# Performance work log

Measured on AMD Instinct MI355X. Metric: run time of the kernel, lower is better.

## Reference

```python
import jax, jax.numpy as jnp
import numpy as np

B, S, D, H = 2, 2048, 2048, 16
HD = D // H
QMAX = 127.0  # 8-bit activation quant


def ste_round(x):
    # forward: round; backward: identity
    return x + jax.lax.stop_gradient(jnp.round(x) - x)


def bitlinear(x, w):
    """BitNet b1.58 linear: per-tensor ternary weights + per-token int8 activations.

    x: [..., in], w: [out, in] -> [..., out]
    """
    w_scale = jnp.maximum(jnp.mean(jnp.abs(w)), 1e-6)
    w_q = jnp.clip(ste_round(w / w_scale), -1.0, 1.0)          # ternary {-1,0,1}
    a_max = jnp.clip(jnp.max(jnp.abs(x), axis=-1, keepdims=True), 1e-8, None)
    x_q = jnp.clip(ste_round(x * (QMAX / a_max)), -QMAX, QMAX)  # int8 range
    y = jnp.einsum('bsi,oi->bso', x_q, w_q)
    return y * (w_scale * a_max / QMAX)


def setup_inputs() -> dict:
    key = jax.random.key(0)
    ks = jax.random.split(key, 5)
    std = 1.0 / np.sqrt(D)  # muP-style init from BitLinear
    return {
        'x': jax.random.normal(ks[0], (B, S, D), dtype=jnp.float32),
        'wq': jax.random.normal(ks[1], (D, D), dtype=jnp.float32) * std,
        'wk': jax.random.normal(ks[2], (D, D), dtype=jnp.float32) * std,
        'wv': jax.random.normal(ks[3], (D, D), dtype=jnp.float32) * std,
        'wo': jax.random.normal(ks[4], (D, D), dtype=jnp.float32) * std,
    }


def reference(x, wq, wk, wv, wo):
    q = bitlinear(x, wq).reshape(B, S, H, HD)
    k = bitlinear(x, wk).reshape(B, S, H, HD)
    v = bitlinear(x, wv).reshape(B, S, H, HD)
    scores = jnp.einsum('bqhd,bkhd->bhqk', q, k) / np.sqrt(HD)
    # causal mask
    causal = jnp.tril(jnp.ones((S, S), dtype=bool))
    scores = jnp.where(causal[None, None], scores, jnp.finfo(scores.dtype).min)
    attn = jax.nn.softmax(scores, axis=-1)
    ctx = jnp.einsum('bhqk,bkhd->bqhd', attn, v).reshape(B, S, D)
    return bitlinear(ctx, wo)
```

## Files before the change

kernel.cpp:

```cpp
#include <hip/hip_runtime.h>
#include <hip/hip_bf16.h>
#include <cstdint>
#include <cstddef>


#define BB 2
#define SS 2048
#define DD 2048
#define HH 16
#define HDD 128
#define MM (BB*SS)

typedef __attribute__((ext_vector_type(8))) short bf16x8;
typedef __attribute__((ext_vector_type(4))) float f32x4;
typedef __attribute__((ext_vector_type(16))) float f32x16;
typedef __attribute__((ext_vector_type(4))) int   i32x4;
typedef unsigned short u16;
typedef unsigned int   u32;
typedef unsigned char  u8;
typedef signed char    s8;

#define MFMA(a,b,c)   __builtin_amdgcn_mfma_f32_16x16x32_bf16(a,b,c,0,0,0)
#define MFMA32(a,b,c) __builtin_amdgcn_mfma_f32_32x32x16_bf16(a,b,c,0,0,0)
#define MFMAI8(a,b,c) __builtin_amdgcn_mfma_i32_16x16x64_i8(a,b,c,0,0,0)

static __device__ __forceinline__ u16 f2bf(float f) {
  u32 x = __float_as_uint(f);
  u32 r = x + 0x7fffu + ((x >> 16) & 1u);
  return (u16)(r >> 16);
}

static __device__ __forceinline__ void gl_lds16(const void* g, void* l) {
  __builtin_amdgcn_global_load_lds((const __attribute__((address_space(1))) void*)g,
                                   (__attribute__((address_space(3))) void*)l, 16, 0, 0);
}

__global__ void k_wabs_partial(const float* __restrict__ w0, const float* __restrict__ w1,
                               const float* __restrict__ w2, const float* __restrict__ w3,
                               double* __restrict__ part) {
  int m = blockIdx.x >> 8, blk = blockIdx.x & 255;
  const float* w = (m == 0) ? w0 : (m == 1) ? w1 : (m == 2) ? w2 : w3;
  const float* p = w + (size_t)blk * 16384;
  double s = 0.0;
  for (int i = threadIdx.x * 4; i < 16384; i += 1024) {
    float4 v = *(const float4*)(p + i);
    s += (double)fabsf(v.x) + (double)fabsf(v.y) + (double)fabsf(v.z) + (double)fabsf(v.w);
  }
  __shared__ double red[256];
  red[threadIdx.x] = s;
  __syncthreads();
  for (int off = 128; off > 0; off >>= 1) {
    if ((int)threadIdx.x < off) red[threadIdx.x] += red[threadIdx.x + off];
    __syncthreads();
  }
  if (threadIdx.x == 0) part[m * 256 + blk] = red[0];
}

__global__ void k_wscale_final(const double* __restrict__ part, float* __restrict__ scales) {
  int m = threadIdx.x;
  if (m < 4) {
    double s = 0.0;
    for (int i = 0; i < 256; i++) s += part[m * 256 + i];
    float v = (float)(s * (1.0 / 4194304.0));
    scales[m] = fmaxf(v, 1e-6f);
  }
}

__global__ void k_wquant(const float* __restrict__ w0, const float* __restrict__ w1,
                         const float* __restrict__ w2, const float* __restrict__ w3,
                         s8* __restrict__ wq, const float* __restrict__ scales) {
  int m = blockIdx.y;
  const float* w = (m == 0) ? w0 : (m == 1) ? w1 : (m == 2) ? w2 : w3;
  float ws = scales[m];
  size_t i = ((size_t)blockIdx.x * 256 + threadIdx.x) * 4;
  float4 v = *(const float4*)(w + i);
  s8 o[4];
  o[0] = (s8)(int)fminf(1.f, fmaxf(-1.f, rintf(v.x / ws)));
  o[1] = (s8)(int)fminf(1.f, fmaxf(-1.f, rintf(v.y / ws)));
  o[2] = (s8)(int)fminf(1.f, fmaxf(-1.f, rintf(v.z / ws)));
  o[3] = (s8)(int)fminf(1.f, fmaxf(-1.f, rintf(v.w / ws)));
  *(int*)(wq + (size_t)m * DD * DD + i) = *(const int*)o;
}

__global__ __launch_bounds__(256) void k_rowquant(const float* __restrict__ x, s8* __restrict__ xq,
                                                  float* __restrict__ amax) {
  int row = blockIdx.x, t = threadIdx.x;
  const float* p = x + (size_t)row * DD + t * 8;
  float4 v0 = *(const float4*)(p);
  float4 v1 = *(const float4*)(p + 4);
  float m = fmaxf(fmaxf(fmaxf(fabsf(v0.x), fabsf(v0.y)), fmaxf(fabsf(v0.z), fabsf(v0.w))),
                  fmaxf(fmaxf(fabsf(v1.x), fabsf(v1.y)), fmaxf(fabsf(v1.z), fabsf(v1.w))));
  m = fmaxf(m, __shfl_xor(m, 1));  m = fmaxf(m, __shfl_xor(m, 2));
  m = fmaxf(m, __shfl_xor(m, 4));  m = fmaxf(m, __shfl_xor(m, 8));
  m = fmaxf(m, __shfl_xor(m, 16)); m = fmaxf(m, __shfl_xor(m, 32));
  __shared__ float red[4];
  if ((t & 63) == 0) red[t >> 6] = m;
  __syncthreads();
  m = fmaxf(fmaxf(red[0], red[1]), fmaxf(red[2], red[3]));
  m = fmaxf(m, 1e-8f);
  if (t == 0) amax[row] = m;
  float s = 127.0f / m;
  s8 o[8];
  o[0] = (s8)(int)fminf(127.f, fmaxf(-127.f, rintf(v0.x * s)));
  o[1] = (s8)(int)fminf(127.f, fmaxf(-127.f, rintf(v0.y * s)));
  o[2] = (s8)(int)fminf(127.f, fmaxf(-127.f, rintf(v0.z * s)));
  o[3] = (s8)(int)fminf(127.f, fmaxf(-127.f, rintf(v0.w * s)));
  o[4] = (s8)(int)fminf(127.f, fmaxf(-127.f, rintf(v1.x * s)));
  o[5] = (s8)(int)fminf(127.f, fmaxf(-127.f, rintf(v1.y * s)));
  o[6] = (s8)(int)fminf(127.f, fmaxf(-127.f, rintf(v1.z * s)));
  o[7] = (s8)(int)fminf(127.f, fmaxf(-127.f, rintf(v1.w * s)));
  *(uint2*)(xq + (size_t)row * DD + t * 8) = *(const uint2*)o;
}

template<bool OB, int NBNL>
__global__ __launch_bounds__(512) void k_gemm(const s8* __restrict__ A, const s8* __restrict__ Bw,
                                              const float* __restrict__ amax,
                                              const float* __restrict__ scales, int sbase,
                                              void* __restrict__ outv) {
  __shared__ alignas(16) u8 Asm[2][128 * 128];
  __shared__ alignas(16) u8 Bsm[2][256 * 128];
  int id = blockIdx.x;
  int xcd = id & 7, kk = id >> 3;
  int bm = kk & 31, bn = xcd * NBNL + (kk >> 5);
  int t = threadIdx.x, w = t >> 6, l = t & 63;
  int wr = w >> 2, wc = w & 3;
  int l15 = l & 15, lh = l >> 4;
  int r0 = t >> 3;
  int c0 = ((t & 7) ^ (r0 & 7)) * 16;
  const s8* Ab = A  + (size_t)(bm * 128) * DD;
  const s8* Bb = Bw + (size_t)(bn * 256) * DD;

#define STG_A(tt) do { u8* d_ = &Asm[(tt) & 1][0];                                    \
    gl_lds16(Ab + (size_t)r0 * DD + (tt) * 128 + c0,        d_ + t * 16);             \
    gl_lds16(Ab + (size_t)(r0 + 64) * DD + (tt) * 128 + c0, d_ + (512 + t) * 16); } while (0)
#define STG_B(tt, h_) do { u8* d_ = &Bsm[(tt) & 1][(h_) * 16384];                     \
    gl_lds16(Bb + (size_t)((h_) * 128 + r0) * DD + (tt) * 128 + c0,        d_ + t * 16);\
    gl_lds16(Bb + (size_t)((h_) * 128 + r0 + 64) * DD + (tt) * 128 + c0,   d_ + (512 + t) * 16); } while (0)

  i32x4 acc[4][4] = {};
  STG_A(0); STG_B(0, 0); STG_B(0, 1); STG_B(1, 0);
  asm volatile("s_waitcnt vmcnt(2)" ::: "memory");
  asm volatile("s_barrier" ::: "memory");
  for (int kb = 0; kb < 16; kb++) {
    int b = kb & 1;
    const u8* Ac = &Asm[b][0];
    const u8* Bc = &Bsm[b][0];
    i32x4 af[4][2], bf[2][2];
    #pragma unroll
    for (int i = 0; i < 4; i++)
      #pragma unroll
      for (int ks = 0; ks < 2; ks++)
        af[i][ks] = *(const i32x4*)(Ac + (wr * 64 + i * 16 + l15) * 128 + (((ks * 4 + lh) ^ (l15 & 7)) * 16));
    #pragma unroll
    for (int j = 0; j < 2; j++)
      #pragma unroll
      for (int ks = 0; ks < 2; ks++)
        bf[j][ks] = *(const i32x4*)(Bc + ((wc + 4 * j) * 16 + l15) * 128 + (((ks * 4 + lh) ^ (l15 & 7)) * 16));
    if (kb + 1 < 16) { STG_A(kb + 1); STG_B(kb + 1, 1); }
    asm volatile("s_barrier" ::: "memory");
    asm volatile("s_waitcnt lgkmcnt(0)" ::: "memory");
    __builtin_amdgcn_sched_barrier(0);
    __builtin_amdgcn_s_setprio(1);
    #pragma unroll
    for (int ks = 0; ks < 2; ks++)
      #pragma unroll
      for (int i = 0; i < 4; i++)
        #pragma unroll
        for (int j = 0; j < 2; j++)
          acc[i][j] = MFMAI8(af[i][ks], bf[j][ks], acc[i][j]);
    __builtin_amdgcn_s_setprio(0);
    asm volatile("s_barrier" ::: "memory");
    i32x4 bg[2][2];
    #pragma unroll
    for (int j = 0; j < 2; j++)
      #pragma unroll
      for (int ks = 0; ks < 2; ks++)
        bg[j][ks] = *(const i32x4*)(Bc + ((wc + 4 * (2 + j)) * 16 + l15) * 128 + (((ks * 4 + lh) ^ (l15 & 7)) * 16));
    if (kb + 2 < 16) STG_B(kb + 2, 0);
    asm volatile("s_barrier" ::: "memory");
    asm volatile("s_waitcnt lgkmcnt(0)" ::: "memory");
    __builtin_amdgcn_sched_barrier(0);
    __builtin_amdgcn_s_setprio(1);
    #pragma unroll
    for (int ks = 0; ks < 2; ks++)
      #pragma unroll
      for (int i = 0; i < 4; i++)
        #pragma unroll
        for (int j = 0; j < 2; j++)
          acc[i][2 + j] = MFMAI8(af[i][ks], bg[j][ks], acc[i][2 + j]);
    __builtin_amdgcn_s_setprio(0);
    if (kb < 14) {
      asm volatile("s_waitcnt vmcnt(2)" ::: "memory");
      asm volatile("s_barrier" ::: "memory");
    } else if (kb == 14) {
      asm volatile("s_waitcnt vmcnt(0)" ::: "memory");
      asm volatile("s_barrier" ::: "memory");
    }
  }
#undef STG_A
#undef STG_B
  int mz = OB ? (bn >> 3) : 0;
  int lcol0 = OB ? ((bn & 7) * 256) : (bn * 256);
  float wsc = scales[sbase + mz];
  u16*   outb = (u16*)outv + (size_t)mz * MM * DD;
  float* outf = (float*)outv;
  #pragma unroll
  for (int i = 0; i < 4; i++) {
    int row0 = bm * 128 + wr * 64 + i * 16 + lh * 4;
    #pragma unroll
    for (int r = 0; r < 4; r++) {
      float sc = (wsc * amax[row0 + r]) / 127.0f;
      #pragma unroll
      for (int j = 0; j < 4; j++) {
        int col = lcol0 + (wc + 4 * j) * 16 + l15;
        float y = (float)acc[i][j][r] * sc;
        if (OB) outb[(size_t)(row0 + r) * DD + col] = f2bf(y);
        else    outf[(size_t)(row0 + r) * DD + col] = y;
      }
    }
  }
}

__global__ __launch_bounds__(256) void k_vtrans(const u16* __restrict__ v, u16* __restrict__ vt) {
  __shared__ u16 tile[64][72];
  int sb = blockIdx.x;
  int db = blockIdx.y;
  int bh = blockIdx.z;
  int b = bh >> 4, h = bh & 15;
  int t = threadIdx.x;
  int ls = t >> 2, ld0 = (t & 3) * 16;
  const u16* src = v + (size_t)(b * SS + sb * 64 + ls) * DD + h * HDD + db * 64 + ld0;
  *(int4*)(&tile[ls][ld0])     = *(const int4*)(src);
  *(int4*)(&tile[ls][ld0 + 8]) = *(const int4*)(src + 8);
  __syncthreads();
  int d = t >> 2, s0 = (t & 3) * 16;
  u16 tmp[16];
  #pragma unroll
  for (int k = 0; k < 16; k++) tmp[k] = tile[s0 + k][d];
  u16* dst = vt + (size_t)((bh * HDD) + db * 64 + d) * SS + sb * 64 + s0;
  *(int4*)(dst)     = *(const int4*)(tmp);
  *(int4*)(dst + 8) = *(const int4*)(tmp + 8);
}

__global__ __launch_bounds__(128) void k_attn(const u16* __restrict__ Q, const u16* __restrict__ K,
                                              const u16* __restrict__ VT, float* __restrict__ O) {
  __shared__ u16 Ks[64 * 128];
  __shared__ u16 Vs[128 * 64];
  __shared__ u16 Ps[2 * 32 * 64];
  int id = blockIdx.x;
  int xcd = id & 7, rr = id >> 3;
  int bh = xcd * 4 + (rr & 3), pr = rr >> 2;
  int b = bh >> 4, h = bh & 15;
  int t = threadIdx.x, w = t >> 6, l = t & 63;
  int l31 = l & 31, hi = l >> 5;
  int l15 = l & 15, lh = l >> 4;
  size_t base = (size_t)(b * SS) * DD + h * HDD;
  const u16* vtb = VT + (size_t)bh * HDD * SS;
  u16* Ptw = Ps + w * 2048;
  const float sc = 0.08838834764831845f;
  int ksr[8], kso[8], vsr[8], vso[8];
  #pragma unroll
  for (int i = 0; i < 8; i++) {
    int s = i * 128 + t;
    ksr[i] = s >> 4; kso[i] = ((s & 15) ^ (ksr[i] & 15)) * 8;
    vsr[i] = s >> 3; vso[i] = ((s & 7) ^ (vsr[i] & 7)) * 8;
  }
  for (int half = 0; half < 2; half++) {
    int qt = half ? (31 - pr) : pr;
    int qrow = qt * 64 + w * 32 + l31;
    bf16x8 qf[8];
    #pragma unroll
    for (int kt = 0; kt < 8; kt++)
      qf[kt] = *(const bf16x8*)(Q + base + (size_t)qrow * DD + kt * 16 + hi * 8);
    f32x4 cacc[2][8] = {};
    float mrun = -INFINITY, lrun = 0.f;
    for (int kb = 0; kb <= qt; kb++) {
      #pragma unroll
      for (int i = 0; i < 8; i++)
        gl_lds16(K + base + (size_t)(kb * 64 + ksr[i]) * DD + kso[i], Ks + (i * 128 + t) * 8);
      #pragma unroll
      for (int i = 0; i < 8; i++)
        gl_lds16(vtb + (size_t)vsr[i] * SS + kb * 64 + vso[i], Vs + (i * 128 + t) * 8);
      __syncthreads();
      f32x16 c0 = {}, c1 = {};
      #pragma unroll
      for (int kt = 0; kt < 8; kt++) {
        int sl = (((kt * 2 + hi) ^ (l31 & 15)) * 8);
        bf16x8 kf0 = *(const bf16x8*)(Ks + l31 * 128 + sl);
        bf16x8 kf1 = *(const bf16x8*)(Ks + (32 + l31) * 128 + sl);
        c0 = MFMA32(kf0, qf[kt], c0);
        c1 = MFMA32(kf1, qf[kt], c1);
      }
      if (kb == qt) {
        #pragma unroll
        for (int rg = 0; rg < 16; rg++) {
          int kv0 = kb * 64 + (rg & 3) + 8 * (rg >> 2) + 4 * hi;
          if (kv0 > qrow)      c0[rg] = -1e30f;
          if (kv0 + 32 > qrow) c1[rg] = -1e30f;
        }
      }
      float ta[16];
      #pragma unroll
      for (int rg = 0; rg < 16; rg++) ta[rg] = fmaxf(c0[rg], c1[rg]);
      #pragma unroll
      for (int off = 8; off > 0; off >>= 1)
        #pragma unroll
        for (int rg = 0; rg < 8; rg++)
          if (rg < off) ta[rg] = fmaxf(ta[rg], ta[rg + off]);
      float pmax = fmaxf(ta[0], __shfl_xor(ta[0], 32));
      if (__any(pmax - mrun > 90.50967f)) {
        float mnew = fmaxf(mrun, pmax);
        float alpha = __expf((mrun - mnew) * sc);
        lrun *= alpha;
        #pragma unroll
        for (int m16 = 0; m16 < 2; m16++)
          #pragma unroll
          for (int r = 0; r < 4; r++) {
            float ar = __shfl(alpha, m16 * 16 + lh * 4 + r);
            #pragma unroll
            for (int n2 = 0; n2 < 8; n2++) cacc[m16][n2][r] *= ar;
          }
        mrun = mnew;
      }
      float msc = mrun * sc;
      float ts[16];
      #pragma unroll
      for (int rg = 0; rg < 16; rg++) {
        float p0 = __expf(fmaf(c0[rg], sc, -msc)); c0[rg] = p0;
        float p1 = __expf(fmaf(c1[rg], sc, -msc)); c1[rg] = p1;
        ts[rg] = p0 + p1;
      }
      #pragma unroll
      for (int off = 8; off > 0; off >>= 1)
        #pragma unroll
        for (int rg = 0; rg < 8; rg++)
          if (rg < off) ts[rg] += ts[rg + off];
      lrun += ts[0] + __shfl_xor(ts[0], 32);
      #pragma unroll
      for (int q4 = 0; q4 < 4; q4++) {
        uint2 pk0, pk1;
        pk0.x = (u32)f2bf(c0[4 * q4 + 0]) | ((u32)f2bf(c0[4 * q4 + 1]) << 16);
        pk0.y = (u32)f2bf(c0[4 * q4 + 2]) | ((u32)f2bf(c0[4 * q4 + 3]) << 16);
        pk1.x = (u32)f2bf(c1[4 * q4 + 0]) | ((u32)f2bf(c1[4 * q4 + 1]) << 16);
        pk1.y = (u32)f2bf(c1[4 * q4 + 2]) | ((u32)f2bf(c1[4 * q4 + 3]) << 16);
        *(uint2*)(Ptw + l31 * 64 + ((q4 ^ (l31 & 7)) * 8 + 4 * hi))       = pk0;
        *(uint2*)(Ptw + l31 * 64 + (((4 + q4) ^ (l31 & 7)) * 8 + 4 * hi)) = pk1;
      }
      #pragma unroll
      for (int ks = 0; ks < 2; ks++) {
        int so = ((ks * 4 + lh) ^ (l15 & 7)) * 8;
        bf16x8 pf0 = *(const bf16x8*)(Ptw + (l15) * 64 + so);
        bf16x8 pf1 = *(const bf16x8*)(Ptw + (16 + l15) * 64 + so);
        #pragma unroll
        for (int n2 = 0; n2 < 8; n2++) {
          bf16x8 vf = *(const bf16x8*)(Vs + (n2 * 16 + l15) * 64 + so);
          cacc[0][n2] = MFMA(pf0, vf, cacc[0][n2]);
          cacc[1][n2] = MFMA(pf1, vf, cacc[1][n2]);
        }
      }
      __syncthreads();
    }
    float inv = 1.0f / lrun;
    #pragma unroll
    for (int m16 = 0; m16 < 2; m16++)
      #pragma unroll
      for (int r = 0; r < 4; r++) {
        float ir = __shfl(inv, m16 * 16 + lh * 4 + r);
        float* op = O + base + (size_t)(qt * 64 + w * 32 + m16 * 16 + lh * 4 + r) * DD;
        #pragma unroll
        for (int n2 = 0; n2 < 8; n2++)
          op[n2 * 16 + l15] = cacc[m16][n2][r] * ir;
      }
  }
}

extern "C" void kernel_launch(void* const* d_in, const int* in_sizes, int n_in,
                              void* d_out, int out_size, void* d_ws, size_t ws_size,
                              hipStream_t stream) {
  const float* x  = (const float*)d_in[0];
  const float* wq = (const float*)d_in[1];
  const float* wk = (const float*)d_in[2];
  const float* wv = (const float*)d_in[3];
  const float* wo = (const float*)d_in[4];
  char* ws = (char*)d_ws;
  float*  scales = (float*)(ws + 0);
  double* part   = (double*)(ws + 256);
  float*  amaxx  = (float*)(ws + 16384);
  float*  amaxc  = (float*)(ws + 49152);
  s8*     wqq    = (s8*)(ws + 131072);
  s8*     xq     = (s8*)(ws + 33685504);
  u16*    vt16   = (u16*)(ws + 33685504);
  u16*    qb     = (u16*)(ws + 50462720);
  u16*    kb     = (u16*)(ws + 67239936);
  u16*    vb     = (u16*)(ws + 84017152);
  float*  ctx    = (float*)(ws + 100794368);
  (void)in_sizes; (void)n_in; (void)out_size; (void)ws_size;

  k_wabs_partial<<<1024, 256, 0, stream>>>(wq, wk, wv, wo, part);
  k_wscale_final<<<1, 64, 0, stream>>>(part, scales);
  k_wquant<<<dim3(4096, 4), 256, 0, stream>>>(wq, wk, wv, wo, wqq, scales);
  k_rowquant<<<MM, 256, 0, stream>>>(x, xq, amaxx);
  k_gemm<true, 3><<<768, 512, 0, stream>>>(xq, wqq, amaxx, scales, 0, (void*)qb);
  k_vtrans<<<dim3(32, 2, 32), 256, 0, stream>>>(vb, vt16);
  k_attn<<<512, 128, 0, stream>>>(qb, kb, vt16, ctx);
  k_rowquant<<<MM, 256, 0, stream>>>(ctx, xq, amaxc);
  k_gemm<false, 1><<<256, 512, 0, stream>>>(xq, wqq + (size_t)3 * DD * DD, amaxc, scales, 3, d_out);
}
```

Measured before the change: 231.6 us.

## Restructure attention to single-wave blocks with double-buffered async K/V loads

The attention kernel now runs one 64-lane wave per block on 32-row query tiles and 32-key blocks, launching twice as many blocks. K and V tiles are double-buffered in LDS, with the next tile's global-to-LDS loads issued before computing on the current one and vmcnt waits replacing block barriers. This aims to overlap memory latency with MFMA work and to remove __syncthreads. In exchange each key step does less MFMA work per load and tiles are smaller, which may lower reuse of K/V across query rows.

```diff
diff --git a/kernel.cpp b/kernel.cpp
--- a/kernel.cpp
+++ b/kernel.cpp
@@ -242,66 +242,79 @@
   *(int4*)(dst + 8) = *(const int4*)(tmp + 8);
 }
 
-__global__ __launch_bounds__(128) void k_attn(const u16* __restrict__ Q, const u16* __restrict__ K,
-                                              const u16* __restrict__ VT, float* __restrict__ O) {
-  __shared__ u16 Ks[64 * 128];
-  __shared__ u16 Vs[128 * 64];
-  __shared__ u16 Ps[2 * 32 * 64];
+__global__ __launch_bounds__(64) void k_attn(const u16* __restrict__ Q, const u16* __restrict__ K,
+                                             const u16* __restrict__ VT, float* __restrict__ O) {
+  __shared__ alignas(16) u16 Ks[2][32 * 128];
+  __shared__ alignas(16) u16 Vs[2][128 * 32];
+  __shared__ alignas(16) u16 Ps[32 * 32];
   int id = blockIdx.x;
   int xcd = id & 7, rr = id >> 3;
   int bh = xcd * 4 + (rr & 3), pr = rr >> 2;
   int b = bh >> 4, h = bh & 15;
-  int t = threadIdx.x, w = t >> 6, l = t & 63;
+  int l = threadIdx.x;
   int l31 = l & 31, hi = l >> 5;
   int l15 = l & 15, lh = l >> 4;
   size_t base = (size_t)(b * SS) * DD + h * HDD;
   const u16* vtb = VT + (size_t)bh * HDD * SS;
-  u16* Ptw = Ps + w * 2048;
   const float sc = 0.08838834764831845f;
-  int ksr[8], kso[8], vsr[8], vso[8];
+  int koff[8];
   #pragma unroll
   for (int i = 0; i < 8; i++) {
-    int s = i * 128 + t;
-    ksr[i] = s >> 4; kso[i] = ((s & 15) ^ (ksr[i] & 15)) * 8;
-    vsr[i] = s >> 3; vso[i] = ((s & 7) ^ (vsr[i] & 7)) * 8;
-  }
+    int row = i * 4 + (l >> 4);
+    koff[i] = row * DD + (((l & 15) ^ (row & 15)) * 8);
+  }
+  int vcol = (((l & 3) ^ ((l >> 3) & 3)) * 8);
+  int vrow0 = l >> 2;
+
+#define ASTAGE(kb_, bf_) do {                                                          \
+    const u16* kp_ = K + base + (size_t)(kb_) * 32 * DD;                               \
+    _Pragma("unroll")                                                                  \
+    for (int i_ = 0; i_ < 8; i_++)                                                     \
+      gl_lds16(kp_ + koff[i_], &Ks[bf_][(i_ * 64 + l) * 8]);                           \
+    const u16* vp_ = vtb + (kb_) * 32 + vcol;                                          \
+    _Pragma("unroll")                                                                  \
+    for (int i_ = 0; i_ < 8; i_++)                                                     \
+      gl_lds16(vp_ + (size_t)(i_ * 16 + vrow0) * SS, &Vs[bf_][(i_ * 64 + l) * 8]);     \
+  } while (0)
+
   for (int half = 0; half < 2; half++) {
-    int qt = half ? (31 - pr) : pr;
-    int qrow = qt * 64 + w * 32 + l31;
+    int qt = half ? (63 - pr) : pr;
+    int qrow = qt * 32 + l31;
     bf16x8 qf[8];
     #pragma unroll
     for (int kt = 0; kt < 8; kt++)
       qf[kt] = *(const bf16x8*)(Q + base + (size_t)qrow * DD + kt * 16 + hi * 8);
     f32x4 cacc[2][8] = {};
     float mrun = -INFINITY, lrun = 0.f;
-    for (int kb = 0; kb <= qt; kb++) {
-      #pragma unroll
-      for (int i = 0; i < 8; i++)
-        gl_lds16(K + base + (size_t)(kb * 64 + ksr[i]) * DD + kso[i], Ks + (i * 128 + t) * 8);
-      #pragma unroll
-      for (int i = 0; i < 8; i++)
-        gl_lds16(vtb + (size_t)vsr[i] * SS + kb * 64 + vso[i], Vs + (i * 128 + t) * 8);
-      __syncthreads();
-      f32x16 c0 = {}, c1 = {};
+    int nkb = qt + 1;
+    ASTAGE(0, 0);
+    for (int kb = 0; kb < nkb; kb++) {
+      int cur = kb & 1;
+      if (kb + 1 < nkb) {
+        ASTAGE(kb + 1, cur ^ 1);
+        asm volatile("s_waitcnt vmcnt(16)" ::: "memory");
+      } else {
+        asm volatile("s_waitcnt vmcnt(0)" ::: "memory");
+      }
+      const u16* Kc = &Ks[cur][0];
+      const u16* Vc = &Vs[cur][0];
+      f32x16 c0 = {};
       #pragma unroll
       for (int kt = 0; kt < 8; kt++) {
         int sl = (((kt * 2 + hi) ^ (l31 & 15)) * 8);
-        bf16x8 kf0 = *(const bf16x8*)(Ks + l31 * 128 + sl);
-        bf16x8 kf1 = *(const bf16x8*)(Ks + (32 + l31) * 128 + sl);
-        c0 = MFMA32(kf0, qf[kt], c0);
-        c1 = MFMA32(kf1, qf[kt], c1);
+        bf16x8 kf = *(const bf16x8*)(Kc + l31 * 128 + sl);
+        c0 = MFMA32(kf, qf[kt], c0);
       }
       if (kb == qt) {
         #pragma unroll
         for (int rg = 0; rg < 16; rg++) {
-          int kv0 = kb * 64 + (rg & 3) + 8 * (rg >> 2) + 4 * hi;
-          if (kv0 > qrow)      c0[rg] = -1e30f;
-          if (kv0 + 32 > qrow) c1[rg] = -1e30f;
+          int kv0 = kb * 32 + (rg & 3) + 8 * (rg >> 2) + 4 * hi;
+          if (kv0 > qrow) c0[rg] = -1e30f;
         }
       }
       float ta[16];
       #pragma unroll
-      for (int rg = 0; rg < 16; rg++) ta[rg] = fmaxf(c0[rg], c1[rg]);
+      for (int rg = 0; rg < 16; rg++) ta[rg] = c0[rg];
       #pragma unroll
       for (int off = 8; off > 0; off >>= 1)
         #pragma unroll
@@ -316,7 +329,7 @@
         for (int m16 = 0; m16 < 2; m16++)
           #pragma unroll
           for (int r = 0; r < 4; r++) {
-            float ar = __shfl(alpha, m16 * 16 + lh * 4 + r);
+            float ar = __shfl(alpha, m16 * 16 + (lh & 3) * 4 + r);
             #pragma unroll
             for (int n2 = 0; n2 < 8; n2++) cacc[m16][n2][r] *= ar;
           }
@@ -327,8 +340,7 @@
       #pragma unroll
       for (int rg = 0; rg < 16; rg++) {
         float p0 = __expf(fmaf(c0[rg], sc, -msc)); c0[rg] = p0;
-        float p1 = __expf(fmaf(c1[rg], sc, -msc)); c1[rg] = p1;
-        ts[rg] = p0 + p1;
+        ts[rg] = p0;
       }
       #pragma unroll
       for (int off = 8; off > 0; off >>= 1)
@@ -338,40 +350,36 @@
       lrun += ts[0] + __shfl_xor(ts[0], 32);
       #pragma unroll
       for (int q4 = 0; q4 < 4; q4++) {
-        uint2 pk0, pk1;
+        uint2 pk0;
         pk0.x = (u32)f2bf(c0[4 * q4 + 0]) | ((u32)f2bf(c0[4 * q4 + 1]) << 16);
         pk0.y = (u32)f2bf(c0[4 * q4 + 2]) | ((u32)f2bf(c0[4 * q4 + 3]) << 16);
-        pk1.x = (u32)f2bf(c1[4 * q4 + 0]) | ((u32)f2bf(c1[4 * q4 + 1]) << 16);
-        pk1.y = (u32)f2bf(c1[4 * q4 + 2]) | ((u32)f2bf(c1[4 * q4 + 3]) << 16);
-        *(uint2*)(Ptw + l31 * 64 + ((q4 ^ (l31 & 7)) * 8 + 4 * hi))       = pk0;
-        *(uint2*)(Ptw + l31 * 64 + (((4 + q4) ^ (l31 & 7)) * 8 + 4 * hi)) = pk1;
-      }
-      #pragma unroll
-      for (int ks = 0; ks < 2; ks++) {
-        int so = ((ks * 4 + lh) ^ (l15 & 7)) * 8;
-        bf16x8 pf0 = *(const bf16x8*)(Ptw + (l15) * 64 + so);
-        bf16x8 pf1 = *(const bf16x8*)(Ptw + (16 + l15) * 64 + so);
+        *(uint2*)(Ps + l31 * 32 + ((q4 ^ ((l31 >> 1) & 3)) * 8 + 4 * hi)) = pk0;
+      }
+      {
+        int so = ((lh ^ ((l15 >> 1) & 3)) * 8);
+        bf16x8 pf0 = *(const bf16x8*)(Ps + (l15) * 32 + so);
+        bf16x8 pf1 = *(const bf16x8*)(Ps + (16 + l15) * 32 + so);
         #pragma unroll
         for (int n2 = 0; n2 < 8; n2++) {
-          bf16x8 vf = *(const bf16x8*)(Vs + (n2 * 16 + l15) * 64 + so);
+          bf16x8 vf = *(const bf16x8*)(Vc + (n2 * 16 + l15) * 32 + so);
           cacc[0][n2] = MFMA(pf0, vf, cacc[0][n2]);
           cacc[1][n2] = MFMA(pf1, vf, cacc[1][n2]);
         }
       }
-      __syncthreads();
     }
     float inv = 1.0f / lrun;
     #pragma unroll
     for (int m16 = 0; m16 < 2; m16++)
       #pragma unroll
       for (int r = 0; r < 4; r++) {
-        float ir = __shfl(inv, m16 * 16 + lh * 4 + r);
-        float* op = O + base + (size_t)(qt * 64 + w * 32 + m16 * 16 + lh * 4 + r) * DD;
+        float ir = __shfl(inv, m16 * 16 + (lh & 3) * 4 + r);
+        float* op = O + base + (size_t)(qt * 32 + m16 * 16 + (lh & 3) * 4 + r) * DD;
         #pragma unroll
         for (int n2 = 0; n2 < 8; n2++)
           op[n2 * 16 + l15] = cacc[m16][n2][r] * ir;
       }
   }
+#undef ASTAGE
 }
 
 extern "C" void kernel_launch(void* const* d_in, const int* in_sizes, int n_in,
@@ -402,7 +410,7 @@
   k_rowquant<<<MM, 256, 0, stream>>>(x, xq, amaxx);
   k_gemm<true, 3><<<768, 512, 0, stream>>>(xq, wqq, amaxx, scales, 0, (void*)qb);
   k_vtrans<<<dim3(32, 2, 32), 256, 0, stream>>>(vb, vt16);
-  k_attn<<<512, 128, 0, stream>>>(qb, kb, vt16, ctx);
+  k_attn<<<1024, 64, 0, stream>>>(qb, kb, vt16, ctx);
   k_rowquant<<<MM, 256, 0, stream>>>(ctx, xq, amaxc);
   k_gemm<false, 1><<<256, 512, 0, stream>>>(xq, wqq + (size_t)3 * DD * DD, amaxc, scales, 3, d_out);
 }
```

New measurement: 256.1 us. 1.11x slower.
